# Kernel tuning notes

Hardware: AMD Instinct MI355X
Metric: run time of the kernel (lower is better)

The kernel has to match this reference:

```python
import jax, jax.numpy as jnp
import numpy as np

K_HOPS = 10
ALPHA = 0.1
N_NODES = 50000
N_EDGES = 600000
F_IN = 128
HIDDEN = 64
N_CLASSES = 40


def setup_inputs() -> dict:
    key = jax.random.key(0)
    k1, k2, k3, k4 = jax.random.split(key, 4)
    x = jax.random.normal(k1, (N_NODES, F_IN), dtype=jnp.float32)
    edge_index = jax.random.randint(k2, (2, N_EDGES), 0, N_NODES, dtype=jnp.int32)
    edge_weight = jnp.ones((N_EDGES,), dtype=jnp.float32)
    W1 = jax.random.normal(k3, (F_IN, HIDDEN), dtype=jnp.float32) * (1.0 / np.sqrt(F_IN))
    b1 = jnp.zeros((HIDDEN,), dtype=jnp.float32)
    W2 = jax.random.normal(k4, (HIDDEN, N_CLASSES), dtype=jnp.float32) * (1.0 / np.sqrt(HIDDEN))
    b2 = jnp.zeros((N_CLASSES,), dtype=jnp.float32)
    return {"x": x, "edge_index": edge_index, "edge_weight": edge_weight,
            "W1": W1, "b1": b1, "W2": W2, "b2": b2}


def reference(x, edge_index, edge_weight, W1, b1, W2, b2):
    n = x.shape[0]
    # GCN symmetric normalization with self-loops (tfg gcn cache)
    self_idx = jnp.arange(n, dtype=edge_index.dtype)
    row = jnp.concatenate([edge_index[0], self_idx])
    col = jnp.concatenate([edge_index[1], self_idx])
    w = jnp.concatenate([edge_weight, jnp.ones((n,), dtype=edge_weight.dtype)])
    deg = jax.ops.segment_sum(w, row, num_segments=n)
    dinv = jnp.where(deg > 0, jax.lax.rsqrt(jnp.maximum(deg, 1e-12)), 0.0)
    nw = dinv[row] * w * dinv[col]  # [E+N] normalized edge weights

    def prop(h):
        # h_out[i] = sum_{(i,j)} nw * h[j]
        return jax.ops.segment_sum(h[col] * nw[:, None], row, num_segments=n)

    def step(h, _):
        h_next = prop(h)
        return h_next, None

    # SSGC: out = (1-alpha)/K * sum_{l=1..K} T^l x + alpha * x
    def step_acc(carry, _):
        h, acc = carry
        h_next = prop(h)
        return (h_next, acc + h_next), None

    (_, acc), _ = jax.lax.scan(step_acc, (x, jnp.zeros_like(x)), None, length=K_HOPS)
    h = (1.0 - ALPHA) / K_HOPS * acc + ALPHA * x  # [N, F]

    h = jax.nn.relu(h @ W1 + b1)  # [N, HIDDEN]
    logits = h @ W2 + b2          # [N, N_CLASSES]
    return logits
```

## Files before the change

kernel.cpp:

```cpp
#include <hip/hip_runtime.h>
#include <hip/hip_fp16.h>
#include <math.h>

constexpr int   N   = 50000;
constexpr int   E   = 600000;
constexpr int   FIN = 128;
constexpr int   H   = 64;
constexpr int   C   = 40;
constexpr int   K   = 10;
constexpr float CK  = (1.0f - 0.1f) / 10.0f;
constexpr float AL  = 0.1f;

typedef float v2f __attribute__((ext_vector_type(2)));

#define XCC_ID_SIMM ((31 << 11) | 20)

__device__ __forceinline__ unsigned pack_fp8x4(float f0, float f1, float f2, float f3) {
    unsigned r = __builtin_amdgcn_cvt_pk_fp8_f32(f0, f1, 0u, false);
    r = __builtin_amdgcn_cvt_pk_fp8_f32(f2, f3, r, true);
    return r;
}

__device__ __forceinline__ float ep_w(unsigned v) {
    return __half2float(__ushort_as_half((unsigned short)(v >> 16)));
}
__device__ __forceinline__ unsigned ep_pack(int c, float w) {
    return (unsigned)(unsigned short)c |
           ((unsigned)__half_as_ushort(__float2half_rn(w)) << 16);
}

__device__ __forceinline__ void accum4(float* s, unsigned v, float w) {
    v2f p0 = __builtin_amdgcn_cvt_pk_f32_fp8(v, false);
    v2f p1 = __builtin_amdgcn_cvt_pk_f32_fp8(v, true);
    s[0] = fmaf(w, p0.x, s[0]); s[1] = fmaf(w, p0.y, s[1]);
    s[2] = fmaf(w, p1.x, s[2]); s[3] = fmaf(w, p1.y, s[3]);
}

constexpr int G1N  = 64;
constexpr int XPAD = 132;
__global__ __launch_bounds__(256, 2) void k_gemm1(const float* __restrict__ x,
                                                  const float* __restrict__ W1,
                                                  float* __restrict__ y0,
                                                  unsigned char* __restrict__ y0f8) {
    __shared__ float ws[FIN * H];
    __shared__ float xs[G1N * XPAD];
    const float4* W14 = (const float4*)W1;
    const float4* x4  = (const float4*)x;
    int t = threadIdx.x;
    int node0 = blockIdx.x * G1N;
    for (int i = t; i < FIN * H / 4; i += 256) ((float4*)ws)[i] = W14[i];
    for (int p = 0; p < 8; ++p) {
        int idx = p * 256 + t;
        int n   = idx >> 5;
        int kk  = idx & 31;
        int node = node0 + n;
        float4 v = (node < N) ? x4[(size_t)node * (FIN / 4) + kk]
                              : make_float4(0.f, 0.f, 0.f, 0.f);
        *(float4*)(xs + n * XPAD + kk * 4) = v;
    }
    __syncthreads();
    int nb = (t >> 4) * 4;
    int cb = (t & 15) * 4;
    float a00=0,a01=0,a02=0,a03=0, a10=0,a11=0,a12=0,a13=0;
    float a20=0,a21=0,a22=0,a23=0, a30=0,a31=0,a32=0,a33=0;
#pragma unroll 8
    for (int k = 0; k < FIN; ++k) {
        float4 wv = *(const float4*)(ws + k * H + cb);
        float x0 = xs[(nb + 0) * XPAD + k];
        float x1 = xs[(nb + 1) * XPAD + k];
        float x2 = xs[(nb + 2) * XPAD + k];
        float x3 = xs[(nb + 3) * XPAD + k];
        a00 = fmaf(x0, wv.x, a00); a01 = fmaf(x0, wv.y, a01);
        a02 = fmaf(x0, wv.z, a02); a03 = fmaf(x0, wv.w, a03);
        a10 = fmaf(x1, wv.x, a10); a11 = fmaf(x1, wv.y, a11);
        a12 = fmaf(x1, wv.z, a12); a13 = fmaf(x1, wv.w, a13);
        a20 = fmaf(x2, wv.x, a20); a21 = fmaf(x2, wv.y, a21);
        a22 = fmaf(x2, wv.z, a22); a23 = fmaf(x2, wv.w, a23);
        a30 = fmaf(x3, wv.x, a30); a31 = fmaf(x3, wv.y, a31);
        a32 = fmaf(x3, wv.z, a32); a33 = fmaf(x3, wv.w, a33);
    }
    float4 rows[4] = {make_float4(a00,a01,a02,a03), make_float4(a10,a11,a12,a13),
                      make_float4(a20,a21,a22,a23), make_float4(a30,a31,a32,a33)};
#pragma unroll
    for (int i = 0; i < 4; ++i) {
        int node = node0 + nb + i;
        if (node >= N) break;
        float4 r = rows[i];
        *(float4*)(y0 + (size_t)node * H + cb) = r;
        *(unsigned*)(y0f8 + (size_t)node * H + cb) = pack_fp8x4(r.x, r.y, r.z, r.w);
    }
}

__global__ __launch_bounds__(256) void k_count(const int* __restrict__ row,
                                               int* __restrict__ cnt8,
                                               unsigned short* __restrict__ rank) {
    int e = blockIdx.x * 256 + threadIdx.x;
    if (e >= E) return;
    unsigned copy = __builtin_amdgcn_s_getreg(XCC_ID_SIMM) & 7u;
    int r = row[e];
    int old = atomicAdd(&cnt8[(size_t)copy * N + r], 1);
    rank[e] = (unsigned short)(old | (copy << 13));
}

__global__ __launch_bounds__(1024) void k_scan_blocks(const int* __restrict__ cnt8,
                                                      int* __restrict__ row_ptr,
                                                      int* __restrict__ bsum) {
    __shared__ int s[1024];
    int gid = blockIdx.x * 1024 + threadIdx.x;
    int v = 0;
    if (gid < N) {
#pragma unroll
        for (int c = 0; c < 8; ++c) v += cnt8[(size_t)c * N + gid];
        v = (v + 3) & ~3;
    }
    s[threadIdx.x] = v;
    __syncthreads();
    for (int off = 1; off < 1024; off <<= 1) {
        int t = (threadIdx.x >= off) ? s[threadIdx.x - off] : 0;
        __syncthreads();
        s[threadIdx.x] += t;
        __syncthreads();
    }
    if (gid < N) row_ptr[gid] = s[threadIdx.x] - v;
    if (threadIdx.x == 1023) bsum[blockIdx.x] = s[1023];
}

constexpr int NB = (N + 1023) / 1024;
__global__ __launch_bounds__(1024) void k_addoff(int* __restrict__ row_ptr,
                                                 const int* __restrict__ bsum,
                                                 int* __restrict__ cnt8,
                                                 unsigned* __restrict__ ep) {
    __shared__ int sboff;
    __shared__ int stot;
    if (threadIdx.x < 64) {
        int lane = threadIdx.x;
        int orig = (lane < NB) ? bsum[lane] : 0;
        int v = orig;
        for (int off = 1; off < 64; off <<= 1) {
            int t = __shfl_up(v, off, 64);
            if (lane >= off) v += t;
        }
        if (lane == (int)blockIdx.x) sboff = v - orig;
        if (lane == NB - 1)          stot  = v;
    }
    __syncthreads();
    int gid = blockIdx.x * 1024 + threadIdx.x;
    if (gid < N) {
        int rp = row_ptr[gid] + sboff;
        row_ptr[gid] = rp;
        int off = rp;
        int real = 0;
#pragma unroll
        for (int c = 0; c < 8; ++c) {
            int t = cnt8[(size_t)c * N + gid];
            cnt8[(size_t)c * N + gid] = off;
            off += t;
            real += t;
        }
        int pd = (real + 3) & ~3;
        for (int j = real; j < pd; ++j) ep[rp + j] = 0u;
    }
    if (gid == 0) {
        row_ptr[N] = stot;
        *(uint4*)(ep + stot) = make_uint4(0u, 0u, 0u, 0u);
    }
}

__global__ __launch_bounds__(256) void k_scatter(const int* __restrict__ row,
                                                 const int* __restrict__ col,
                                                 const float* __restrict__ w,
                                                 const unsigned short* __restrict__ rank,
                                                 const int* __restrict__ base8,
                                                 unsigned* __restrict__ ep) {
    int base = blockIdx.x * 1024 + threadIdx.x;
#pragma unroll
    for (int i = 0; i < 4; ++i) {
        int e = base + i * 256;
        if (e < E) {
            unsigned rk = rank[e];
            int copy = rk >> 13;
            int r = row[e];
            int p = base8[(size_t)copy * N + r] + (rk & 0x1FFF);
            ep[p] = ep_pack(col[e], w[e]);
        }
    }
}

__global__ void k_deg_dinv(const unsigned* __restrict__ ep, const int* __restrict__ row_ptr,
                           float* __restrict__ dinv, float* __restrict__ dinv2) {
    int i = blockIdx.x * blockDim.x + threadIdx.x;
    if (i >= N) return;
    float d = 1.0f;
    int e0 = row_ptr[i], e1 = row_ptr[i + 1];
    for (int j = e0; j < e1; ++j) d += ep_w(ep[j]);
    float di = rsqrtf(d);
    dinv[i]  = di;
    dinv2[i] = di * di;
}

__global__ __launch_bounds__(256) void k_norm(unsigned* __restrict__ ep,
                                              const int* __restrict__ row_ptr,
                                              const float* __restrict__ dinv) {
    int node = blockIdx.x * 32 + (threadIdx.x >> 3);
    if (node >= N) return;
    int l = threadIdx.x & 7;
    float dr = dinv[node];
    int e0 = row_ptr[node], e1 = row_ptr[node + 1];
    for (int j = e0 + l; j < e1; j += 8) {
        unsigned v = ep[j];
        int c = v & 0xFFFFu;
        ep[j] = ep_pack(c, ep_w(v) * dr * dinv[c]);
    }
}

constexpr int HSP = 68;
template <bool WRITE_H, bool ACC_INIT, bool FINAL>
__global__ __launch_bounds__(256) void k_prop(const unsigned* __restrict__ hin,
                                              unsigned* __restrict__ hout,
                                              __half* __restrict__ acch,
                                              const float* __restrict__ dinv2,
                                              const int* __restrict__ row_ptr,
                                              const unsigned* __restrict__ ep,
                                              const float4* __restrict__ y04,
                                              const float* __restrict__ b1,
                                              const float* __restrict__ W2,
                                              const float* __restrict__ b2,
                                              float* __restrict__ out) {
    extern __shared__ float smem[];
    float* w2s = smem;
    float* hs  = smem + H * C;
    float* b2s = hs + 16 * HSP;
    float* b1s = b2s + C;
    int t = threadIdx.x;
    if (FINAL) {
        for (int i = t; i < H * C; i += 256) w2s[i] = W2[i];
        if (t < C) b2s[t] = b2[t];
        if (t < H) b1s[t] = b1[t];
        __syncthreads();
    }
    int lane = t & 63;
    int nib  = (t >> 6) * 4 + (lane >> 4);
    int l    = lane & 15;
    int node = blockIdx.x * 16 + nib;
    bool nv  = node < N;
    int nodec = nv ? node : N - 1;
    int start = row_ptr[nodec];
    int pdeg  = nv ? (row_ptr[nodec + 1] - start) : 0;
    int md = pdeg;
#pragma unroll
    for (int off = 16; off <= 32; off <<= 1) md = max(md, __shfl_xor(md, off, 64));

    size_t base = (size_t)nodec * 16 + l;
    unsigned vself = hin[base];
    float d2       = dinv2[nodec];
    uint2* ap = (uint2*)(acch + (size_t)nodec * H + l * 4);
    uint2 old;
    if (nv && (FINAL || !ACC_INIT)) old = *ap;

    float s[4];
#pragma unroll
    for (int i = 0; i < 4; ++i) s[i] = 0.f;

    const unsigned* rp = ep + start;
    uint4 ea = *(const uint4*)rp;
    uint4 eb = *(const uint4*)(rp + ((4 < pdeg) ? 4 : 0));
    for (int batch = 0; batch < md; batch += 8) {
        uint4 ca = ea, cb = eb;
        int n0 = batch + 8, n1 = batch + 12;
        ea = *(const uint4*)(rp + ((n0 < pdeg) ? n0 : 0));
        eb = *(const uint4*)(rp + ((n1 < pdeg) ? n1 : 0));
        unsigned v0 = hin[(size_t)(ca.x & 0xFFFFu) * 16 + l];
        unsigned v1 = hin[(size_t)(ca.y & 0xFFFFu) * 16 + l];
        unsigned v2 = hin[(size_t)(ca.z & 0xFFFFu) * 16 + l];
        unsigned v3 = hin[(size_t)(ca.w & 0xFFFFu) * 16 + l];
        unsigned v4 = hin[(size_t)(cb.x & 0xFFFFu) * 16 + l];
        unsigned v5 = hin[(size_t)(cb.y & 0xFFFFu) * 16 + l];
        unsigned v6 = hin[(size_t)(cb.z & 0xFFFFu) * 16 + l];
        unsigned v7 = hin[(size_t)(cb.w & 0xFFFFu) * 16 + l];
        accum4(s, v0, (batch     < pdeg) ? ep_w(ca.x) : 0.0f);
        accum4(s, v1, (batch + 1 < pdeg) ? ep_w(ca.y) : 0.0f);
        accum4(s, v2, (batch + 2 < pdeg) ? ep_w(ca.z) : 0.0f);
        accum4(s, v3, (batch + 3 < pdeg) ? ep_w(ca.w) : 0.0f);
        accum4(s, v4, (batch + 4 < pdeg) ? ep_w(cb.x) : 0.0f);
        accum4(s, v5, (batch + 5 < pdeg) ? ep_w(cb.y) : 0.0f);
        accum4(s, v6, (batch + 6 < pdeg) ? ep_w(cb.z) : 0.0f);
        accum4(s, v7, (batch + 7 < pdeg) ? ep_w(cb.w) : 0.0f);
    }
    if (nv) {
        accum4(s, vself, d2);
        if (WRITE_H) {
            hout[base] = pack_fp8x4(s[0], s[1], s[2], s[3]);
        }
        if (FINAL) {
            const unsigned* u = (const unsigned*)&old;
#pragma unroll
            for (int d = 0; d < 2; ++d) {
                float2 f = __half22float2(*(__half2*)&u[d]);
                s[2*d+0] += f.x; s[2*d+1] += f.y;
            }
            float4 ya = y04[(size_t)nodec * (H / 4) + l];
            const float* bp = b1s + l * 4;
            float* hp = hs + nib * HSP + l * 4;
            hp[0] = fmaxf(fmaf(CK, s[0], fmaf(AL, ya.x, bp[0])), 0.f);
            hp[1] = fmaxf(fmaf(CK, s[1], fmaf(AL, ya.y, bp[1])), 0.f);
            hp[2] = fmaxf(fmaf(CK, s[2], fmaf(AL, ya.z, bp[2])), 0.f);
            hp[3] = fmaxf(fmaf(CK, s[3], fmaf(AL, ya.w, bp[3])), 0.f);
        } else {
            if (!ACC_INIT) {
                const unsigned* u = (const unsigned*)&old;
#pragma unroll
                for (int d = 0; d < 2; ++d) {
                    float2 f = __half22float2(*(__half2*)&u[d]);
                    s[2*d+0] += f.x; s[2*d+1] += f.y;
                }
            }
            uint2 nvp;
            unsigned* u = (unsigned*)&nvp;
#pragma unroll
            for (int d = 0; d < 2; ++d) {
                __half2 h = __floats2half2_rn(s[2*d+0], s[2*d+1]);
                u[d] = *(unsigned*)&h;
            }
            *ap = nvp;
        }
    }
    if (FINAL) {
        __syncthreads();
        int node0 = blockIdx.x * 16;
        for (int o = t; o < 16 * C; o += 256) {
            int nl = o / C, c = o % C;
            int n2 = node0 + nl;
            if (n2 >= N) continue;
            float v = b2s[c];
            const float* hr = &hs[nl * HSP];
#pragma unroll
            for (int k = 0; k < H; ++k) v = fmaf(hr[k], w2s[k * C + c], v);
            out[n2 * C + c] = v;
        }
    }
}

extern "C" void kernel_launch(void* const* d_in, const int* in_sizes, int n_in,
                              void* d_out, int out_size, void* d_ws, size_t ws_size,
                              hipStream_t stream) {
    const float* x  = (const float*)d_in[0];
    const int*   ei = (const int*)d_in[1];
    const float* ew = (const float*)d_in[2];
    const float* W1 = (const float*)d_in[3];
    const float* b1 = (const float*)d_in[4];
    const float* W2 = (const float*)d_in[5];
    const float* b2 = (const float*)d_in[6];
    float* out = (float*)d_out;

    const int* row = ei;
    const int* col = ei + E;

    char* ws = (char*)d_ws;
    size_t off = 0;
    auto alloc = [&](size_t bytes) -> char* {
        char* p = ws + off;
        off = (off + bytes + 1023) & ~(size_t)1023;
        return p;
    };
    constexpr size_t EPAD = (size_t)E + 3 * (size_t)N + 1024;
    float*          y0   = (float*)alloc((size_t)N * H * 4);
    unsigned char*  y0f8 = (unsigned char*)alloc((size_t)N * H);
    unsigned char*  ha   = (unsigned char*)alloc((size_t)N * H);
    unsigned char*  hb   = (unsigned char*)alloc((size_t)N * H);
    __half*         acch = (__half*)alloc((size_t)N * H * 2);
    int*            cnt8 = (int*)alloc((size_t)8 * N * 4);
    unsigned short* rank = (unsigned short*)alloc((size_t)E * 2);
    float*    dinv   = (float*)   alloc((size_t)N * 4);
    float*    dinv2  = (float*)   alloc((size_t)N * 4);
    int*      row_ptr= (int*)     alloc((size_t)(N + 1) * 4);
    int*      bsum   = (int*)     alloc(64 * 4);
    unsigned* ep     = (unsigned*)alloc(EPAD * 4);

    hipMemsetAsync(cnt8, 0, (size_t)8 * N * 4, stream);

    k_gemm1<<<(N + G1N - 1) / G1N, 256, 0, stream>>>(x, W1, y0, y0f8);

    k_count<<<(E + 255) / 256, 256, 0, stream>>>(row, cnt8, rank);

    k_scan_blocks<<<NB, 1024, 0, stream>>>(cnt8, row_ptr, bsum);
    k_addoff<<<NB, 1024, 0, stream>>>(row_ptr, bsum, cnt8, ep);

    k_scatter<<<(E + 1023) / 1024, 256, 0, stream>>>(row, col, ew, rank, cnt8, ep);
    k_deg_dinv<<<(N + 255) / 256, 256, 0, stream>>>(ep, row_ptr, dinv, dinv2);
    k_norm<<<(N + 31) / 32, 256, 0, stream>>>(ep, row_ptr, dinv);

    const unsigned* hin = (const unsigned*)y0f8;
    unsigned* bufs[2] = {(unsigned*)ha, (unsigned*)hb};
    const float4* y04 = (const float4*)y0;
    int grid = (N + 15) / 16;
    size_t smemF = (size_t)(H * C + 16 * HSP + C + H) * 4;
    for (int hop = 0; hop < K; ++hop) {
        unsigned* hout = bufs[hop & 1];
        if (hop == 0)
            k_prop<true, true, false><<<grid, 256, 0, stream>>>(hin, hout, acch, dinv2,
                row_ptr, ep, y04, b1, W2, b2, out);
        else if (hop == K - 1)
            k_prop<false, false, true><<<grid, 256, smemF, stream>>>(hin, hout, acch, dinv2,
                row_ptr, ep, y04, b1, W2, b2, out);
        else
            k_prop<true, false, false><<<grid, 256, 0, stream>>>(hin, hout, acch, dinv2,
                row_ptr, ep, y04, b1, W2, b2, out);
        hin = hout;
    }
}
```

Before: 291.8 us.

## Build CSR via two-level bucket sort with LDS histograms instead of global atomics

Replaces the per-XCC global-atomic counting and rank-based scatter with a two-pass bucket sort. Pass one bins edges into 64-row buckets using LDS histograms and a scanned bin-by-block offset matrix. Pass two counts and emits within each bucket using LDS atomics, which aims to remove global atomic contention and the memset of the 8-copy counters. It also vectorises the degree and normalisation kernels to uint4 loads with 8 lanes per node, at the cost of more kernel launches and a 64-bit intermediate edge array.

New measurement: 279.9 us. 1.04x faster.

```diff
diff --git a/kernel.cpp b/kernel.cpp
--- a/kernel.cpp
+++ b/kernel.cpp
@@ -11,9 +11,12 @@
 constexpr float CK  = (1.0f - 0.1f) / 10.0f;
 constexpr float AL  = 0.1f;
 
+constexpr int NBIN = (N + 63) / 64;
+constexpr int HB   = (E + 1023) / 1024;
+constexpr int M    = NBIN * HB;
+constexpr int SB   = (M + 1023) / 1024;
+
 typedef float v2f __attribute__((ext_vector_type(2)));
-
-#define XCC_ID_SIMM ((31 << 11) | 20)
 
 __device__ __forceinline__ unsigned pack_fp8x4(float f0, float f1, float f2, float f3) {
     unsigned r = __builtin_amdgcn_cvt_pk_fp8_f32(f0, f1, 0u, false);
@@ -91,28 +94,116 @@
     }
 }
 
-__global__ __launch_bounds__(256) void k_count(const int* __restrict__ row,
-                                               int* __restrict__ cnt8,
-                                               unsigned short* __restrict__ rank) {
-    int e = blockIdx.x * 256 + threadIdx.x;
-    if (e >= E) return;
-    unsigned copy = __builtin_amdgcn_s_getreg(XCC_ID_SIMM) & 7u;
-    int r = row[e];
-    int old = atomicAdd(&cnt8[(size_t)copy * N + r], 1);
-    rank[e] = (unsigned short)(old | (copy << 13));
-}
-
-__global__ __launch_bounds__(1024) void k_scan_blocks(const int* __restrict__ cnt8,
+__global__ __launch_bounds__(256) void k_hist(const int* __restrict__ row,
+                                              unsigned* __restrict__ bhT) {
+    __shared__ unsigned h[NBIN];
+    for (int i = threadIdx.x; i < NBIN; i += 256) h[i] = 0;
+    __syncthreads();
+    int b = blockIdx.x;
+    int base = b * 1024 + threadIdx.x;
+#pragma unroll
+    for (int i = 0; i < 4; ++i) {
+        int e = base + i * 256;
+        if (e < E) atomicAdd(&h[row[e] >> 6], 1u);
+    }
+    __syncthreads();
+    for (int i = threadIdx.x; i < NBIN; i += 256)
+        bhT[(size_t)i * HB + b] = h[i];
+}
+
+__global__ __launch_bounds__(1024) void k_scan1(unsigned* __restrict__ S,
+                                                unsigned* __restrict__ bsumA) {
+    __shared__ unsigned s[1024];
+    int gid = blockIdx.x * 1024 + threadIdx.x;
+    unsigned v = (gid < M) ? S[gid] : 0;
+    s[threadIdx.x] = v;
+    __syncthreads();
+    for (int off = 1; off < 1024; off <<= 1) {
+        unsigned t = (threadIdx.x >= off) ? s[threadIdx.x - off] : 0;
+        __syncthreads();
+        s[threadIdx.x] += t;
+        __syncthreads();
+    }
+    if (gid < M) S[gid] = s[threadIdx.x] - v;
+    if (threadIdx.x == 1023) bsumA[blockIdx.x] = s[1023];
+}
+
+__global__ __launch_bounds__(512) void k_scan2(unsigned* __restrict__ bsumA) {
+    __shared__ unsigned s[512];
+    int t = threadIdx.x;
+    unsigned v = (t < SB) ? bsumA[t] : 0;
+    s[t] = v;
+    __syncthreads();
+    for (int off = 1; off < 512; off <<= 1) {
+        unsigned x = (t >= off) ? s[t - off] : 0;
+        __syncthreads();
+        s[t] += x;
+        __syncthreads();
+    }
+    if (t < SB) bsumA[t] = s[t] - v;
+}
+
+__global__ __launch_bounds__(256) void k_bucket(const int* __restrict__ row,
+                                                const int* __restrict__ col,
+                                                const float* __restrict__ w,
+                                                const unsigned* __restrict__ S,
+                                                const unsigned* __restrict__ bofs,
+                                                unsigned long long* __restrict__ barr) {
+    __shared__ unsigned cur[NBIN];
+    int b = blockIdx.x;
+    for (int i = threadIdx.x; i < NBIN; i += 256) {
+        unsigned idx = (unsigned)i * HB + (unsigned)b;
+        cur[i] = S[idx] + bofs[idx >> 10];
+    }
+    __syncthreads();
+    int base = b * 1024 + threadIdx.x;
+#pragma unroll
+    for (int i = 0; i < 4; ++i) {
+        int e = base + i * 256;
+        if (e < E) {
+            int r = row[e];
+            unsigned p = atomicAdd(&cur[r >> 6], 1u);
+            unsigned short wh = __half_as_ushort(__float2half_rn(w[e]));
+            barr[p] = ((unsigned long long)wh << 32) |
+                      ((unsigned long long)(unsigned)r << 16) |
+                      (unsigned long long)(unsigned)col[e];
+        }
+    }
+}
+
+__device__ __forceinline__ unsigned bucket_lo(const unsigned* S, const unsigned* bofs,
+                                              int bin) {
+    unsigned idx = (unsigned)bin * HB;
+    return S[idx] + bofs[idx >> 10];
+}
+
+__global__ __launch_bounds__(256) void k_cnt(const unsigned long long* __restrict__ barr,
+                                             const unsigned* __restrict__ S,
+                                             const unsigned* __restrict__ bofs,
+                                             int* __restrict__ cnt) {
+    __shared__ unsigned rc[64];
+    if (threadIdx.x < 64) rc[threadIdx.x] = 0;
+    __syncthreads();
+    int bin = blockIdx.x;
+    unsigned i0 = bucket_lo(S, bofs, bin);
+    unsigned i1 = (bin + 1 < NBIN) ? bucket_lo(S, bofs, bin + 1) : (unsigned)E;
+    for (unsigned i = i0 + threadIdx.x; i < i1; i += 256) {
+        unsigned r = (unsigned)(barr[i] >> 16) & 0xFFFFu;
+        atomicAdd(&rc[r & 63], 1u);
+    }
+    __syncthreads();
+    int r0 = bin * 64;
+    if (threadIdx.x < 64 && r0 + (int)threadIdx.x < N)
+        cnt[r0 + threadIdx.x] = (int)rc[threadIdx.x];
+}
+
+__global__ __launch_bounds__(1024) void k_scan_blocks(const int* __restrict__ cnt,
                                                       int* __restrict__ row_ptr,
                                                       int* __restrict__ bsum) {
     __shared__ int s[1024];
     int gid = blockIdx.x * 1024 + threadIdx.x;
     int v = 0;
-    if (gid < N) {
-#pragma unroll
-        for (int c = 0; c < 8; ++c) v += cnt8[(size_t)c * N + gid];
-        v = (v + 3) & ~3;
-    }
+    if (gid < N) v = (cnt[gid] + 3) & ~3;
     s[threadIdx.x] = v;
     __syncthreads();
     for (int off = 1; off < 1024; off <<= 1) {
@@ -128,7 +219,7 @@
 constexpr int NB = (N + 1023) / 1024;
 __global__ __launch_bounds__(1024) void k_addoff(int* __restrict__ row_ptr,
                                                  const int* __restrict__ bsum,
-                                                 int* __restrict__ cnt8,
+                                                 const int* __restrict__ cnt,
                                                  unsigned* __restrict__ ep) {
     __shared__ int sboff;
     __shared__ int stot;
@@ -148,15 +239,7 @@
     if (gid < N) {
         int rp = row_ptr[gid] + sboff;
         row_ptr[gid] = rp;
-        int off = rp;
-        int real = 0;
-#pragma unroll
-        for (int c = 0; c < 8; ++c) {
-            int t = cnt8[(size_t)c * N + gid];
-            cnt8[(size_t)c * N + gid] = off;
-            off += t;
-            real += t;
-        }
+        int real = cnt[gid];
         int pd = (real + 3) & ~3;
         for (int j = real; j < pd; ++j) ep[rp + j] = 0u;
     }
@@ -166,36 +249,51 @@
     }
 }
 
-__global__ __launch_bounds__(256) void k_scatter(const int* __restrict__ row,
-                                                 const int* __restrict__ col,
-                                                 const float* __restrict__ w,
-                                                 const unsigned short* __restrict__ rank,
-                                                 const int* __restrict__ base8,
-                                                 unsigned* __restrict__ ep) {
-    int base = blockIdx.x * 1024 + threadIdx.x;
-#pragma unroll
-    for (int i = 0; i < 4; ++i) {
-        int e = base + i * 256;
-        if (e < E) {
-            unsigned rk = rank[e];
-            int copy = rk >> 13;
-            int r = row[e];
-            int p = base8[(size_t)copy * N + r] + (rk & 0x1FFF);
-            ep[p] = ep_pack(col[e], w[e]);
-        }
-    }
-}
-
-__global__ void k_deg_dinv(const unsigned* __restrict__ ep, const int* __restrict__ row_ptr,
-                           float* __restrict__ dinv, float* __restrict__ dinv2) {
-    int i = blockIdx.x * blockDim.x + threadIdx.x;
-    if (i >= N) return;
-    float d = 1.0f;
-    int e0 = row_ptr[i], e1 = row_ptr[i + 1];
-    for (int j = e0; j < e1; ++j) d += ep_w(ep[j]);
-    float di = rsqrtf(d);
-    dinv[i]  = di;
-    dinv2[i] = di * di;
+__global__ __launch_bounds__(256) void k_emit(const unsigned long long* __restrict__ barr,
+                                              const unsigned* __restrict__ S,
+                                              const unsigned* __restrict__ bofs,
+                                              const int* __restrict__ row_ptr,
+                                              unsigned* __restrict__ ep) {
+    __shared__ unsigned cur[64];
+    int bin = blockIdx.x;
+    int r0 = bin * 64;
+    if (threadIdx.x < 64) {
+        int r = r0 + (int)threadIdx.x;
+        cur[threadIdx.x] = (r < N) ? (unsigned)row_ptr[r] : 0u;
+    }
+    __syncthreads();
+    unsigned i0 = bucket_lo(S, bofs, bin);
+    unsigned i1 = (bin + 1 < NBIN) ? bucket_lo(S, bofs, bin + 1) : (unsigned)E;
+    for (unsigned i = i0 + threadIdx.x; i < i1; i += 256) {
+        unsigned long long v = barr[i];
+        unsigned r = (unsigned)(v >> 16) & 0xFFFFu;
+        unsigned p = atomicAdd(&cur[r & 63], 1u);
+        ep[p] = (unsigned)(v & 0xFFFFu) | (((unsigned)(v >> 32) & 0xFFFFu) << 16);
+    }
+}
+
+__global__ __launch_bounds__(256) void k_deg_dinv(const unsigned* __restrict__ ep,
+                                                  const int* __restrict__ row_ptr,
+                                                  float* __restrict__ dinv,
+                                                  float* __restrict__ dinv2) {
+    int node = blockIdx.x * 32 + (threadIdx.x >> 3);
+    if (node >= N) return;
+    int l = threadIdx.x & 7;
+    int e0 = row_ptr[node], e1 = row_ptr[node + 1];
+    float d = 0.f;
+    for (int j4 = (e0 >> 2) + l; j4 * 4 < e1; j4 += 8) {
+        uint4 v = ((const uint4*)ep)[j4];
+        d += ep_w(v.x) + ep_w(v.y) + ep_w(v.z) + ep_w(v.w);
+    }
+    d += __shfl_xor(d, 1, 64);
+    d += __shfl_xor(d, 2, 64);
+    d += __shfl_xor(d, 4, 64);
+    if (l == 0) {
+        d += 1.0f;
+        float di = rsqrtf(d);
+        dinv[node]  = di;
+        dinv2[node] = di * di;
+    }
 }
 
 __global__ __launch_bounds__(256) void k_norm(unsigned* __restrict__ ep,
@@ -206,10 +304,13 @@
     int l = threadIdx.x & 7;
     float dr = dinv[node];
     int e0 = row_ptr[node], e1 = row_ptr[node + 1];
-    for (int j = e0 + l; j < e1; j += 8) {
-        unsigned v = ep[j];
-        int c = v & 0xFFFFu;
-        ep[j] = ep_pack(c, ep_w(v) * dr * dinv[c]);
+    for (int j4 = (e0 >> 2) + l; j4 * 4 < e1; j4 += 8) {
+        uint4 v = ((uint4*)ep)[j4];
+        v.x = ep_pack(v.x & 0xFFFFu, ep_w(v.x) * dr * dinv[v.x & 0xFFFFu]);
+        v.y = ep_pack(v.y & 0xFFFFu, ep_w(v.y) * dr * dinv[v.y & 0xFFFFu]);
+        v.z = ep_pack(v.z & 0xFFFFu, ep_w(v.z) * dr * dinv[v.z & 0xFFFFu]);
+        v.w = ep_pack(v.w & 0xFFFFu, ep_w(v.w) * dr * dinv[v.w & 0xFFFFu]);
+        ((uint4*)ep)[j4] = v;
     }
 }
 
@@ -363,30 +464,34 @@
         return p;
     };
     constexpr size_t EPAD = (size_t)E + 3 * (size_t)N + 1024;
-    float*          y0   = (float*)alloc((size_t)N * H * 4);
-    unsigned char*  y0f8 = (unsigned char*)alloc((size_t)N * H);
-    unsigned char*  ha   = (unsigned char*)alloc((size_t)N * H);
-    unsigned char*  hb   = (unsigned char*)alloc((size_t)N * H);
-    __half*         acch = (__half*)alloc((size_t)N * H * 2);
-    int*            cnt8 = (int*)alloc((size_t)8 * N * 4);
-    unsigned short* rank = (unsigned short*)alloc((size_t)E * 2);
-    float*    dinv   = (float*)   alloc((size_t)N * 4);
-    float*    dinv2  = (float*)   alloc((size_t)N * 4);
-    int*      row_ptr= (int*)     alloc((size_t)(N + 1) * 4);
-    int*      bsum   = (int*)     alloc(64 * 4);
-    unsigned* ep     = (unsigned*)alloc(EPAD * 4);
-
-    hipMemsetAsync(cnt8, 0, (size_t)8 * N * 4, stream);
+    float*              y0    = (float*)alloc((size_t)N * H * 4);
+    unsigned char*      y0f8  = (unsigned char*)alloc((size_t)N * H);
+    unsigned char*      ha    = (unsigned char*)alloc((size_t)N * H);
+    unsigned char*      hb    = (unsigned char*)alloc((size_t)N * H);
+    __half*             acch  = (__half*)alloc((size_t)N * H * 2);
+    int*                cnt   = (int*)alloc((size_t)N * 4);
+    unsigned*           bhT   = (unsigned*)alloc((size_t)M * 4);
+    unsigned*           bsumA = (unsigned*)alloc(512 * 4);
+    unsigned long long* barr  = (unsigned long long*)alloc((size_t)E * 8);
+    float*    dinv    = (float*)alloc((size_t)N * 4);
+    float*    dinv2   = (float*)alloc((size_t)N * 4);
+    int*      row_ptr = (int*)alloc((size_t)(N + 1) * 4);
+    int*      bsum    = (int*)alloc(64 * 4);
+    unsigned* ep      = (unsigned*)alloc(EPAD * 4);
 
     k_gemm1<<<(N + G1N - 1) / G1N, 256, 0, stream>>>(x, W1, y0, y0f8);
 
-    k_count<<<(E + 255) / 256, 256, 0, stream>>>(row, cnt8, rank);
-
-    k_scan_blocks<<<NB, 1024, 0, stream>>>(cnt8, row_ptr, bsum);
-    k_addoff<<<NB, 1024, 0, stream>>>(row_ptr, bsum, cnt8, ep);
-
-    k_scatter<<<(E + 1023) / 1024, 256, 0, stream>>>(row, col, ew, rank, cnt8, ep);
-    k_deg_dinv<<<(N + 255) / 256, 256, 0, stream>>>(ep, row_ptr, dinv, dinv2);
+    k_hist  <<<HB, 256, 0, stream>>>(row, bhT);
+    k_scan1 <<<SB, 1024, 0, stream>>>(bhT, bsumA);
+    k_scan2 <<<1, 512, 0, stream>>>(bsumA);
+    k_bucket<<<HB, 256, 0, stream>>>(row, col, ew, bhT, bsumA, barr);
+    k_cnt   <<<NBIN, 256, 0, stream>>>(barr, bhT, bsumA, cnt);
+
+    k_scan_blocks<<<NB, 1024, 0, stream>>>(cnt, row_ptr, bsum);
+    k_addoff<<<NB, 1024, 0, stream>>>(row_ptr, bsum, cnt, ep);
+
+    k_emit<<<NBIN, 256, 0, stream>>>(barr, bhT, bsumA, row_ptr, ep);
+    k_deg_dinv<<<(N + 31) / 32, 256, 0, stream>>>(ep, row_ptr, dinv, dinv2);
     k_norm<<<(N + 31) / 32, 256, 0, stream>>>(ep, row_ptr, dinv);
 
     const unsigned* hin = (const unsigned*)y0f8;
```
